# Optimization experiments

Measured on AMD Instinct MI355X. Metric: run time of the kernel, lower is better.

Reference implementation:

```python
import jax, jax.numpy as jnp
import numpy as np

N_NODES = 50000
N_EDGES = 800000
IN_F = 256
OUT_F = 64
ALPHA = 0.2  # LeakyReLU negative slope


def setup_inputs() -> dict:
    key = jax.random.key(0)
    k1, k2, k3, k4 = jax.random.split(key, 4)
    h = jax.random.normal(k1, (N_NODES, IN_F), dtype=jnp.float32)
    edge_index = jax.random.randint(k2, (2, N_EDGES), 0, N_NODES, dtype=jnp.int32)
    # xavier_uniform-like scale for params
    W = jax.random.uniform(k3, (IN_F, OUT_F), dtype=jnp.float32, minval=-1.0, maxval=1.0) * (1.414 * np.sqrt(6.0 / (IN_F + OUT_F)))
    a = jax.random.uniform(k4, (2 * OUT_F, 1), dtype=jnp.float32, minval=-1.0, maxval=1.0) * (1.414 * np.sqrt(6.0 / (2 * OUT_F + 1)))
    return {"h": h, "edge_index": edge_index, "W": W, "a": a}


def reference(h, edge_index, W, a):
    src = edge_index[0]  # row index of sparse matrix (softmax dim=1 -> per-row)
    dst = edge_index[1]  # column index -> neighbor whose Wh is aggregated

    Wh = jax.nn.leaky_relu(h @ W, negative_slope=ALPHA)          # [N, F]
    e1 = (Wh @ a[:OUT_F, :])[:, 0]                               # [N]
    e2 = (Wh @ a[OUT_F:, :])[:, 0]                               # [N]
    e = e1[src] + e2[dst]                                        # [E] edge scores

    # sparse softmax over dim=1 (per source/row segment)
    m = jax.ops.segment_max(e, src, num_segments=N_NODES)        # [N]
    e_exp = jnp.exp(e - m[src])                                  # [E]
    denom = jax.ops.segment_sum(e_exp, src, num_segments=N_NODES)  # [N]
    attn = e_exp / denom[src]                                    # [E]

    # sparse-dense matmul: h_prime[i] = sum_{edges with src=i} attn * Wh[dst]
    h_prime = jax.ops.segment_sum(attn[:, None] * Wh[dst], src, num_segments=N_NODES)  # [N, F]

    return jax.nn.elu(h_prime)  # concat=True
```

## Files before the change

### kernel.cpp

```cpp
#include <hip/hip_runtime.h>
#include <hip/hip_bf16.h>
#include <math.h>

#define N_NODES 50000
#define N_EDGES 800000
#define IN_F 256
#define OUT_F 64
#define ALPHA 0.2f

#define NPB 64
#define NBKT 782
#define CAP 1536
#define BIN_EPB 4096
#define BIN_NB 196
#define GEMM_NB 391

typedef __attribute__((ext_vector_type(8))) short short8;
typedef __attribute__((ext_vector_type(8))) unsigned short u16x8;
typedef __attribute__((ext_vector_type(4))) float f32x4;

__device__ __forceinline__ unsigned short f2b(float f) {
    unsigned u = __float_as_uint(f);
    unsigned r = (u + 0x7fffu + ((u >> 16) & 1u)) >> 16;
    return (unsigned short)r;
}
__device__ __forceinline__ float b2f(unsigned short b) {
    return __uint_as_float(((unsigned)b) << 16);
}
__device__ __forceinline__ unsigned cvt2(float a, float b) {
    __hip_bfloat162 h2 = __float22bfloat162_rn(make_float2(a, b));
    return *reinterpret_cast<unsigned*>(&h2);
}

union abits {
    short8 s8;
    unsigned u[4];
};

__global__ __launch_bounds__(256) void k_wprep(const float* __restrict__ W,
                                               short* __restrict__ Wfrag,
                                               int* __restrict__ gcursor) {
    int idx = blockIdx.x * 256 + threadIdx.x;
    if (idx < NBKT) gcursor[idx] = idx * CAP;
    if (idx >= 8 * 4 * 64 * 8) return;
    int j = idx & 7;
    int l = (idx >> 3) & 63;
    int t = (idx >> 9) & 3;
    int s = idx >> 11;
    int k = s * 32 + (l >> 4) * 8 + j;
    int n = t * 16 + (l & 15);
    Wfrag[idx] = (short)f2b(W[k * OUT_F + n]);
}

__global__ __launch_bounds__(256, 4) void k_bc(
    const float* __restrict__ h, const short* __restrict__ Wfrag,
    const float* __restrict__ a, unsigned short* __restrict__ Whb,
    float* __restrict__ ew, const int* __restrict__ ei,
    int* __restrict__ gcursor, int* __restrict__ binned) {
    __shared__ int bc[NBKT];
    __shared__ short8 wlds[2048];

    if (blockIdx.x < BIN_NB) {
        const int t = threadIdx.x;
        for (int i = t; i < NBKT; i += 256) bc[i] = 0;
        __syncthreads();

        int s[16], d[16];
        const int e0 = blockIdx.x * BIN_EPB;
#pragma unroll
        for (int i = 0; i < 16; ++i) {
            int e = e0 + i * 256 + t;
            if (e < N_EDGES) {
                s[i] = ei[e];
                d[i] = ei[N_EDGES + e];
                atomicAdd(&bc[s[i] >> 6], 1);
            } else {
                s[i] = -1;
            }
        }
        __syncthreads();
        for (int i = t; i < NBKT; i += 256) {
            int cnt = bc[i];
            bc[i] = cnt ? atomicAdd(&gcursor[i], cnt) : 0;
        }
        __syncthreads();
#pragma unroll
        for (int i = 0; i < 16; ++i) {
            if (s[i] >= 0) {
                int bkt = s[i] >> 6;
                int idx = atomicAdd(&bc[bkt], 1);
                if (idx < (bkt + 1) * CAP)
                    binned[idx] = ((s[i] & 63) << 16) | d[i];
            }
        }
        return;
    }

    const int bid = blockIdx.x - BIN_NB;
    const int tid = threadIdx.x;
    const int wid = tid >> 6;
    const int l = tid & 63;
    const int lo = l & 15;
    const int g = l >> 4;
    const int m0 = (bid * 4 + wid) * 32;

    {
        int4* dstv = (int4*)wlds;
        const int4* srcv = (const int4*)Wfrag;
#pragma unroll
        for (int i = 0; i < 8; ++i) dstv[tid + i * 256] = srcv[tid + i * 256];
    }
    __syncthreads();

    const int r0 = m0 + lo;
    const int r1 = m0 + 16 + lo;
    const int r0c = r0 < N_NODES ? r0 : N_NODES - 1;
    const int r1c = r1 < N_NODES ? r1 : N_NODES - 1;

    f32x4 acc[2][4];
#pragma unroll
    for (int mt = 0; mt < 2; ++mt)
#pragma unroll
        for (int t = 0; t < 4; ++t)
            acc[mt][t] = (f32x4){0.f, 0.f, 0.f, 0.f};

#pragma unroll
    for (int s = 0; s < 8; ++s) {
        const float* p0 = &h[(size_t)r0c * IN_F + s * 32 + g * 8];
        const float* p1 = &h[(size_t)r1c * IN_F + s * 32 + g * 8];
        float4 x0 = *(const float4*)p0;
        float4 y0 = *(const float4*)(p0 + 4);
        float4 x1 = *(const float4*)p1;
        float4 y1 = *(const float4*)(p1 + 4);
        abits A0, A1;
        A0.u[0] = cvt2(x0.x, x0.y);
        A0.u[1] = cvt2(x0.z, x0.w);
        A0.u[2] = cvt2(y0.x, y0.y);
        A0.u[3] = cvt2(y0.z, y0.w);
        A1.u[0] = cvt2(x1.x, x1.y);
        A1.u[1] = cvt2(x1.z, x1.w);
        A1.u[2] = cvt2(y1.x, y1.y);
        A1.u[3] = cvt2(y1.z, y1.w);
#pragma unroll
        for (int t = 0; t < 4; ++t) {
            short8 bf = wlds[(s * 4 + t) * 64 + l];
            acc[0][t] = __builtin_amdgcn_mfma_f32_16x16x32_bf16(
                A0.s8, bf, acc[0][t], 0, 0, 0);
            acc[1][t] = __builtin_amdgcn_mfma_f32_16x16x32_bf16(
                A1.s8, bf, acc[1][t], 0, 0, 0);
        }
    }

    float a2v[4];
#pragma unroll
    for (int t = 0; t < 4; ++t) a2v[t] = a[OUT_F + t * 16 + lo];

#pragma unroll
    for (int mt = 0; mt < 2; ++mt) {
        float p[4];
#pragma unroll
        for (int reg = 0; reg < 4; ++reg) {
            float pp = 0.f;
#pragma unroll
            for (int t = 0; t < 4; ++t) {
                float v = acc[mt][t][reg];
                v = v > 0.f ? v : ALPHA * v;
                acc[mt][t][reg] = v;
                pp += v * a2v[t];
            }
            p[reg] = pp;
        }
#pragma unroll
        for (int reg = 0; reg < 4; ++reg) {
#pragma unroll
            for (int mask = 1; mask < 16; mask <<= 1)
                p[reg] += __shfl_xor(p[reg], mask, 64);
        }
        const int rbase = m0 + mt * 16 + g * 4;
        if (lo == 0) {
#pragma unroll
            for (int reg = 0; reg < 4; ++reg)
                if (rbase + reg < N_NODES) ew[rbase + reg] = __expf(p[reg]);
        }
#pragma unroll
        for (int reg = 0; reg < 4; ++reg) {
            int r = rbase + reg;
            if (r < N_NODES) {
#pragma unroll
                for (int t = 0; t < 4; ++t)
                    Whb[(size_t)r * OUT_F + t * 16 + lo] =
                        f2b(acc[mt][t][reg]);
            }
        }
    }
}

__global__ __launch_bounds__(512) void k_fuse(
    const int* __restrict__ binned, const int* __restrict__ gcursor,
    const float* __restrict__ ew, const unsigned short* __restrict__ Whb,
    float* __restrict__ out) {
    __shared__ unsigned short ldst[CAP];
    __shared__ int hist[NPB];
    __shared__ int sstart[NPB];
    const int t = threadIdx.x;
    const int b = blockIdx.x;

    int mycnt = gcursor[b] - b * CAP;
    mycnt = mycnt < 0 ? 0 : (mycnt > CAP ? CAP : mycnt);
    const int rb = b * CAP;

    if (t < NPB) hist[t] = 0;
    __syncthreads();

    int p0 = -1, p1 = -1, p2 = -1;
    if (t < mycnt) {
        p0 = binned[rb + t];
        atomicAdd(&hist[p0 >> 16], 1);
    }
    if (t + 512 < mycnt) {
        p1 = binned[rb + t + 512];
        atomicAdd(&hist[p1 >> 16], 1);
    }
    if (t + 1024 < mycnt) {
        p2 = binned[rb + t + 1024];
        atomicAdd(&hist[p2 >> 16], 1);
    }
    __syncthreads();

    if (t < 64) {
        int my = hist[t];
        int x = my;
#pragma unroll
        for (int o = 1; o < 64; o <<= 1) {
            int u = __shfl_up(x, o, 64);
            if (t >= o) x += u;
        }
        sstart[t] = x - my;
        hist[t] = x - my;
    }
    __syncthreads();

    if (p0 >= 0) ldst[atomicAdd(&hist[p0 >> 16], 1)] = (unsigned short)(p0 & 0xFFFF);
    if (p1 >= 0) ldst[atomicAdd(&hist[p1 >> 16], 1)] = (unsigned short)(p1 & 0xFFFF);
    if (p2 >= 0) ldst[atomicAdd(&hist[p2 >> 16], 1)] = (unsigned short)(p2 & 0xFFFF);
    __syncthreads();

    const int grp = t >> 3;
    const int fl = t & 7;
    const int node = b * NPB + grp;
    const int start = sstart[grp];
    const int end = (grp < NPB - 1) ? sstart[grp + 1] : mycnt;

    float acc[8] = {0.f, 0.f, 0.f, 0.f, 0.f, 0.f, 0.f, 0.f};
    float den = 0.f;
    for (int j = start; j < end; ++j) {
        int dd = (int)ldst[j];
        float w = ew[dd];
        u16x8 wv = *(const u16x8*)&Whb[(size_t)dd * OUT_F + fl * 8];
        den += w;
#pragma unroll
        for (int k = 0; k < 8; ++k) acc[k] += w * b2f(wv[k]);
    }

    if (node < N_NODES) {
        float4 r0, r1;
        if (end > start) {
            float inv = 1.f / den;
            float v;
            v = acc[0] * inv; r0.x = v > 0.f ? v : expm1f(v);
            v = acc[1] * inv; r0.y = v > 0.f ? v : expm1f(v);
            v = acc[2] * inv; r0.z = v > 0.f ? v : expm1f(v);
            v = acc[3] * inv; r0.w = v > 0.f ? v : expm1f(v);
            v = acc[4] * inv; r1.x = v > 0.f ? v : expm1f(v);
            v = acc[5] * inv; r1.y = v > 0.f ? v : expm1f(v);
            v = acc[6] * inv; r1.z = v > 0.f ? v : expm1f(v);
            v = acc[7] * inv; r1.w = v > 0.f ? v : expm1f(v);
        } else {
            r0 = make_float4(0.f, 0.f, 0.f, 0.f);
            r1 = r0;
        }
        *(float4*)&out[(size_t)node * OUT_F + fl * 8] = r0;
        *(float4*)&out[(size_t)node * OUT_F + fl * 8 + 4] = r1;
    }
}

extern "C" void kernel_launch(void* const* d_in, const int* in_sizes, int n_in,
                              void* d_out, int out_size, void* d_ws,
                              size_t ws_size, hipStream_t stream) {
    const float* h = (const float*)d_in[0];
    const int* ei = (const int*)d_in[1];
    const float* W = (const float*)d_in[2];
    const float* a = (const float*)d_in[3];
    float* out = (float*)d_out;

    float* ws = (float*)d_ws;
    unsigned short* Whb = (unsigned short*)ws;
    float* ew = ws + 1600000;
    short* Wfrag = (short*)(ws + 1650000);
    int* gcursor = (int*)(ws + 1658192);
    int* binned = (int*)(ws + 1659216);

    k_wprep<<<64, 256, 0, stream>>>(W, Wfrag, gcursor);
    k_bc<<<BIN_NB + GEMM_NB, 256, 0, stream>>>(h, Wfrag, a, Whb, ew, ei,
                                               gcursor, binned);
    k_fuse<<<NBKT, 512, 0, stream>>>(binned, gcursor, ew, Whb, out);
}
```

Baseline: 49.47 us.

## Drop W-prep kernel: build bf16 W fragments in-kernel, memset cursors, unroll gather

Removes the separate k_wprep launch. Each GEMM block now reads fp32 W directly and converts it to bf16 MFMA fragments in LDS. The bucket cursors are zeroed with hipMemsetAsync and made relative to the bucket, so k_fuse reads the count directly. The gather loop in k_fuse is unrolled by two so more memory loads are in flight. The trade is that every GEMM block redoes the strided W conversion, and a memset node replaces the kernel launch.

```diff
diff --git a/kernel.cpp b/kernel.cpp
--- a/kernel.cpp
+++ b/kernel.cpp
@@ -37,23 +37,8 @@
     unsigned u[4];
 };
 
-__global__ __launch_bounds__(256) void k_wprep(const float* __restrict__ W,
-                                               short* __restrict__ Wfrag,
-                                               int* __restrict__ gcursor) {
-    int idx = blockIdx.x * 256 + threadIdx.x;
-    if (idx < NBKT) gcursor[idx] = idx * CAP;
-    if (idx >= 8 * 4 * 64 * 8) return;
-    int j = idx & 7;
-    int l = (idx >> 3) & 63;
-    int t = (idx >> 9) & 3;
-    int s = idx >> 11;
-    int k = s * 32 + (l >> 4) * 8 + j;
-    int n = t * 16 + (l & 15);
-    Wfrag[idx] = (short)f2b(W[k * OUT_F + n]);
-}
-
 __global__ __launch_bounds__(256, 4) void k_bc(
-    const float* __restrict__ h, const short* __restrict__ Wfrag,
+    const float* __restrict__ h, const float* __restrict__ W,
     const float* __restrict__ a, unsigned short* __restrict__ Whb,
     float* __restrict__ ew, const int* __restrict__ ei,
     int* __restrict__ gcursor, int* __restrict__ binned) {
@@ -81,7 +66,7 @@
         __syncthreads();
         for (int i = t; i < NBKT; i += 256) {
             int cnt = bc[i];
-            bc[i] = cnt ? atomicAdd(&gcursor[i], cnt) : 0;
+            bc[i] = cnt ? i * CAP + atomicAdd(&gcursor[i], cnt) : 0;
         }
         __syncthreads();
 #pragma unroll
@@ -105,10 +90,26 @@
     const int m0 = (bid * 4 + wid) * 32;
 
     {
-        int4* dstv = (int4*)wlds;
-        const int4* srcv = (const int4*)Wfrag;
-#pragma unroll
-        for (int i = 0; i < 8; ++i) dstv[tid + i * 256] = srcv[tid + i * 256];
+#pragma unroll
+        for (int i = 0; i < 8; ++i) {
+            int e = tid + i * 256;
+            int s = e >> 8;
+            int tt = (e >> 6) & 3;
+            int ll = e & 63;
+            int kbase = s * 32 + (ll >> 4) * 8;
+            int n = tt * 16 + (ll & 15);
+            const float* wp = &W[(size_t)kbase * OUT_F + n];
+            float f0 = wp[0 * OUT_F], f1 = wp[1 * OUT_F];
+            float f2 = wp[2 * OUT_F], f3 = wp[3 * OUT_F];
+            float f4 = wp[4 * OUT_F], f5 = wp[5 * OUT_F];
+            float f6 = wp[6 * OUT_F], f7 = wp[7 * OUT_F];
+            abits en;
+            en.u[0] = cvt2(f0, f1);
+            en.u[1] = cvt2(f2, f3);
+            en.u[2] = cvt2(f4, f5);
+            en.u[3] = cvt2(f6, f7);
+            wlds[e] = en.s8;
+        }
     }
     __syncthreads();
 
@@ -205,7 +206,7 @@
     const int t = threadIdx.x;
     const int b = blockIdx.x;
 
-    int mycnt = gcursor[b] - b * CAP;
+    int mycnt = gcursor[b];
     mycnt = mycnt < 0 ? 0 : (mycnt > CAP ? CAP : mycnt);
     const int rb = b * CAP;
 
@@ -253,7 +254,22 @@
 
     float acc[8] = {0.f, 0.f, 0.f, 0.f, 0.f, 0.f, 0.f, 0.f};
     float den = 0.f;
-    for (int j = start; j < end; ++j) {
+    int j = start;
+    for (; j + 2 <= end; j += 2) {
+        int dd0 = (int)ldst[j];
+        int dd1 = (int)ldst[j + 1];
+        float w0 = ew[dd0];
+        float w1 = ew[dd1];
+        u16x8 wv0 = *(const u16x8*)&Whb[(size_t)dd0 * OUT_F + fl * 8];
+        u16x8 wv1 = *(const u16x8*)&Whb[(size_t)dd1 * OUT_F + fl * 8];
+        den += w0 + w1;
+#pragma unroll
+        for (int k = 0; k < 8; ++k) {
+            acc[k] += w0 * b2f(wv0[k]);
+            acc[k] += w1 * b2f(wv1[k]);
+        }
+    }
+    if (j < end) {
         int dd = (int)ldst[j];
         float w = ew[dd];
         u16x8 wv = *(const u16x8*)&Whb[(size_t)dd * OUT_F + fl * 8];
@@ -296,12 +312,11 @@
     float* ws = (float*)d_ws;
     unsigned short* Whb = (unsigned short*)ws;
     float* ew = ws + 1600000;
-    short* Wfrag = (short*)(ws + 1650000);
-    int* gcursor = (int*)(ws + 1658192);
-    int* binned = (int*)(ws + 1659216);
-
-    k_wprep<<<64, 256, 0, stream>>>(W, Wfrag, gcursor);
-    k_bc<<<BIN_NB + GEMM_NB, 256, 0, stream>>>(h, Wfrag, a, Whb, ew, ei,
+    int* gcursor = (int*)(ws + 1650000);
+    int* binned = (int*)(ws + 1651024);
+
+    hipMemsetAsync(gcursor, 0, NBKT * sizeof(int), stream);
+    k_bc<<<BIN_NB + GEMM_NB, 256, 0, stream>>>(h, W, a, Whb, ew, ei,
                                                gcursor, binned);
     k_fuse<<<NBKT, 512, 0, stream>>>(binned, gcursor, ew, Whb, out);
 }
```

Measured after the change: 51.66 us. 1.04x slower.
